# Performance work log

Hardware: AMD Instinct MI355X
Metric: run time of the kernel (lower is better)

## Reference

```python
import jax, jax.numpy as jnp
import numpy as np

N = 2_000_000   # num_nodes
C = 128         # in_channels
B = 256         # num graphs
K = 32          # max branches per graph (branch ids in [0, K))
NEG_SLOPE = 0.01  # torch leaky_relu default


def setup_inputs() -> dict:
    key = jax.random.key(0)
    k1, k2, k3, k4, k5, k6 = jax.random.split(key, 6)
    node_embed = jax.random.normal(k1, (N, C), dtype=jnp.float32)
    batch = jnp.sort(jax.random.randint(k2, (N,), 0, B, dtype=jnp.int64))
    branch = jax.random.randint(k3, (N,), 0, K, dtype=jnp.int64)
    s1 = 1.0 / np.sqrt(C)
    W1 = jax.random.uniform(k4, (C, C), jnp.float32, -s1, s1)
    b1 = jnp.zeros((C,), jnp.float32)
    W2 = jax.random.uniform(k5, (C, 1), jnp.float32, -s1, s1)
    b2 = jnp.zeros((1,), jnp.float32)
    return {"node_embed": node_embed, "batch": batch, "branch": branch,
            "W1": W1, "b1": b1, "W2": W2, "b2": b2}


def reference(node_embed, batch, branch, W1, b1, W2, b2):
    # Original code compacts branch ids via per-graph offsets (cumsum of max+1).
    # Equivalent static-shape formulation: global slot id = batch*K + branch,
    # and a per-graph mask keeping slots b <= max(branch in graph) — exactly the
    # branches 0..num_branch_per_graph-1 that repeat_interleave covers (including
    # empty branches below the max, whose pooled embed is 0 -> MLP(0)).
    gid = batch * K + branch                               # [N]
    branch_embed = jax.ops.segment_sum(node_embed, gid, num_segments=B * K)  # [B*K, C]
    h = branch_embed @ W1 + b1
    h = jnp.where(h >= 0, h, NEG_SLOPE * h)                # leaky_relu
    branch_value = h @ W2 + b2                             # [B*K, 1]
    max_b = jax.ops.segment_max(branch, batch, num_segments=B)  # [B]
    mask = (jnp.arange(K)[None, :] <= max_b[:, None]).astype(branch_value.dtype)  # [B, K]
    graph_value = jnp.sum(branch_value.reshape(B, K) * mask, axis=1, keepdims=True)  # [B, 1]
    return graph_value
```

## Files before the change

kernel.cpp:

```cpp
#include <hip/hip_runtime.h>

#define NCH 128
#define NGR 256
#define NBR 32
#define NEG_SLOPE 0.01f

typedef __attribute__((ext_vector_type(8))) short bf16x8;
typedef __attribute__((ext_vector_type(4))) float f32x4;

constexpr int TROWS = 128;

__device__ inline unsigned short f32_bf16(float x) {
    unsigned u = __float_as_uint(x);
    return (unsigned short)((u + 0x7FFFu + ((u >> 16) & 1u)) >> 16);
}
__device__ inline float bf16_f32(unsigned short h) {
    return __uint_as_float(((unsigned)h) << 16);
}

__global__ __launch_bounds__(1024) void scatter_mfma(
    const float* __restrict__ node_embed,
    const int*   __restrict__ batch,
    const int*   __restrict__ branch,
    float*       __restrict__ branch_embed,
    int*         __restrict__ max_b,
    int n_nodes)
{
    __shared__ float buf[2][TROWS][NCH] __attribute__((aligned(16)));
    __shared__ unsigned short sbr[2][TROWS] __attribute__((aligned(16)));
    __shared__ int seg_s[2];
    __shared__ int wm[2];

    const int t    = threadIdx.x;
    const int g    = blockIdx.x;
    const int wave = t >> 6;
    const int lane = t & 63;
    const int c    = wave >> 1;
    const int p    = wave & 1;

    if (t < 2) {
        const int target = g + t;
        int lo = 0, hi = n_nodes;
        while (lo < hi) { int mid = (lo + hi) >> 1; if (batch[mid] < target) lo = mid + 1; else hi = mid; }
        seg_s[t] = lo;
    }
    __syncthreads();
    const int s0 = seg_s[0], s1 = seg_s[1];
    const int nt = (s1 - s0 + TROWS - 1) / TROWS;

    auto stage_data = [&](int c0n, int nb) {
        #pragma unroll
        for (int u = 0; u < 4; ++u) {
            const int koff = (u * 16 + wave) * 1024;
            const size_t lanebyte = (size_t)koff + (size_t)lane * 16;
            const int rowg = c0n + (int)(lanebyte >> 9);
            const char* src = (const char*)node_embed + (((size_t)c0n << 9) + lanebyte);
            if (rowg >= s1)
                src = (const char*)node_embed + ((size_t)s0 << 9);
            __builtin_amdgcn_global_load_lds(
                (const __attribute__((address_space(1))) void*)src,
                (__attribute__((address_space(3))) void*)((char*)&buf[nb][0][0] + koff),
                16, 0, 0);
        }
    };

    f32x4 acc0 = {0.f, 0.f, 0.f, 0.f};
    f32x4 acc1 = {0.f, 0.f, 0.f, 0.f};
    int mymax = -1;

    if (nt > 0) {
        stage_data(s0, 0);
        if (t < TROWS) {
            const int i = s0 + t;
            unsigned short mm = 0xFFFFu;
            if (i < s1) { const int br = branch[i]; mymax = max(mymax, br); mm = (unsigned short)br; }
            sbr[0][t] = mm;
        }
        __syncthreads();
    }

    const int gq = lane >> 4;
    const int m  = lane & 15;

    for (int ti = 0; ti < nt; ++ti) {
        const int cb = ti & 1;
        const bool pre = (ti + 1 < nt);
        unsigned short nxt = 0xFFFFu;
        if (pre) {
            const int c0n = s0 + (ti + 1) * TROWS;
            stage_data(c0n, cb ^ 1);
            if (t < TROWS) {
                const int i = c0n + t;
                if (i < s1) { const int br = branch[i]; mymax = max(mymax, br); nxt = (unsigned short)br; }
            }
        }

        #pragma unroll
        for (int kk = 0; kk < 2; ++kk) {
            const int rb = (p + 2 * kk) * 32;
            const int4 idraw = *(const int4*)((const char*)&sbr[cb][0] + rb * 2 + gq * 16);
            unsigned idv[8];
            idv[0] = (unsigned)idraw.x & 0xFFFFu; idv[1] = (unsigned)idraw.x >> 16;
            idv[2] = (unsigned)idraw.y & 0xFFFFu; idv[3] = (unsigned)idraw.y >> 16;
            idv[4] = (unsigned)idraw.z & 0xFFFFu; idv[5] = (unsigned)idraw.z >> 16;
            idv[6] = (unsigned)idraw.w & 0xFFFFu; idv[7] = (unsigned)idraw.w >> 16;

            bf16x8 a0, a1, bhi, blo;
            #pragma unroll
            for (int j = 0; j < 8; ++j) {
                const float v = buf[cb][rb + gq * 8 + j][c * 16 + m];
                const unsigned short h = f32_bf16(v);
                const unsigned short l = f32_bf16(v - bf16_f32(h));
                bhi[j] = (short)h;
                blo[j] = (short)l;
                a0[j] = (idv[j] == (unsigned)m)        ? (short)0x3F80 : (short)0;
                a1[j] = (idv[j] == (unsigned)(m + 16)) ? (short)0x3F80 : (short)0;
            }
            acc0 = __builtin_amdgcn_mfma_f32_16x16x32_bf16(a0, bhi, acc0, 0, 0, 0);
            acc0 = __builtin_amdgcn_mfma_f32_16x16x32_bf16(a0, blo, acc0, 0, 0, 0);
            acc1 = __builtin_amdgcn_mfma_f32_16x16x32_bf16(a1, bhi, acc1, 0, 0, 0);
            acc1 = __builtin_amdgcn_mfma_f32_16x16x32_bf16(a1, blo, acc1, 0, 0, 0);
        }

        if (pre && t < TROWS) sbr[cb ^ 1][t] = nxt;
        __syncthreads();
    }

    __syncthreads();
    float* red = &buf[0][0][0];
    if (p == 1) {
        float* dst = red + ((size_t)c * 64 + lane) * 8;
        #pragma unroll
        for (int r = 0; r < 4; ++r) { dst[r] = acc0[r]; dst[4 + r] = acc1[r]; }
    }
    __syncthreads();
    if (p == 0) {
        const float* src = red + ((size_t)c * 64 + lane) * 8;
        #pragma unroll
        for (int r = 0; r < 4; ++r) { acc0[r] += src[r]; acc1[r] += src[4 + r]; }
        const int sr = gq * 4;
        float* be = branch_embed + (size_t)g * NBR * NCH + (size_t)c * 16 + m;
        #pragma unroll
        for (int r = 0; r < 4; ++r) {
            be[(sr + r) * NCH]      = acc0[r];
            be[(16 + sr + r) * NCH] = acc1[r];
        }
    }

    int v = mymax;
    #pragma unroll
    for (int off = 32; off > 0; off >>= 1) v = max(v, __shfl_down(v, off));
    if (wave < 2 && lane == 0) wm[wave] = v;
    __syncthreads();
    if (t == 0) max_b[g] = max(wm[0], wm[1]);
}

__global__ __launch_bounds__(256) void mlp_kernel(
    const float* __restrict__ branch_embed,
    const int*   __restrict__ max_b,
    const float* __restrict__ W1,
    const float* __restrict__ b1,
    const float* __restrict__ W2,
    const float* __restrict__ b2,
    float*       __restrict__ out)
{
    __shared__ float W1s[NCH * NCH];
    __shared__ float b1s[NCH], W2s[NCH];
    __shared__ float rows[2][NCH];
    __shared__ float red[2][NCH];
    __shared__ float sval[NBR];

    const int t = threadIdx.x;
    const int b = blockIdx.x;

    for (int i = t; i < NCH * NCH / 4; i += 256)
        ((float4*)W1s)[i] = ((const float4*)W1)[i];
    if (t < NCH) { b1s[t] = b1[t]; W2s[t] = W2[t]; }
    __syncthreads();

    const int half = t >> 7;
    const int j    = t & 127;

    for (int k0 = 0; k0 < NBR; k0 += 2) {
        const int slot = k0 + half;
        rows[half][j] = branch_embed[((size_t)b * NBR + slot) * NCH + j];
        __syncthreads();

        float h = b1s[j];
        #pragma unroll 8
        for (int i = 0; i < NCH; ++i)
            h += rows[half][i] * W1s[i * NCH + j];
        h = (h >= 0.0f) ? h : NEG_SLOPE * h;
        red[half][j] = h * W2s[j];
        __syncthreads();

        for (int off = 64; off > 0; off >>= 1) {
            if (j < off) red[half][j] += red[half][j + off];
            __syncthreads();
        }
        if (j == 0) sval[slot] = red[half][0];
        __syncthreads();
    }

    if (t < 64) {
        const int mb = max_b[b];
        float v = (t < NBR && t <= mb) ? (sval[t] + b2[0]) : 0.0f;
        #pragma unroll
        for (int off = 32; off > 0; off >>= 1) v += __shfl_down(v, off);
        if (t == 0) out[b] = v;
    }
}

extern "C" void kernel_launch(void* const* d_in, const int* in_sizes, int n_in,
                              void* d_out, int out_size, void* d_ws, size_t ws_size,
                              hipStream_t stream) {
    const float* node_embed = (const float*)d_in[0];
    const int*   batch      = (const int*)d_in[1];
    const int*   branch     = (const int*)d_in[2];
    const float* W1         = (const float*)d_in[3];
    const float* b1         = (const float*)d_in[4];
    const float* W2         = (const float*)d_in[5];
    const float* b2         = (const float*)d_in[6];
    float*       out        = (float*)d_out;

    const int n_nodes = in_sizes[0] / NCH;

    float* branch_embed = (float*)d_ws;
    int*   max_b = (int*)((char*)d_ws + (size_t)NGR * NBR * NCH * sizeof(float));

    scatter_mfma<<<NGR, 1024, 0, stream>>>(node_embed, batch, branch,
                                           branch_embed, max_b, n_nodes);
    mlp_kernel<<<NGR, 256, 0, stream>>>(branch_embed, max_b, W1, b1, W2, b2, out);
}
```

Before: 246.1 us.

## Deepen scatter pipeline to two tiles ahead with async branch-id loads

Restructures the scatter kernel's tile loop so two tiles are in flight. The branch ids are now also loaded straight into LDS with global_load_lds, and waits use explicit vmcnt counters and raw barriers instead of __syncthreads. The bf16 high part becomes a cheap truncation rather than round-to-nearest. Tail rows are masked in a templated compute path, and every wave folds the max branch into its own mymax. The aim is to hide global-load latency and cut per-tile register/ALU overhead. The cost is fragile hand-tuned waitcnt counts and some extra reduction work.

Result: faster. 235.9 us (-4.2%).

```diff
diff --git a/kernel.cpp b/kernel.cpp
--- a/kernel.cpp
+++ b/kernel.cpp
@@ -10,12 +10,49 @@
 
 constexpr int TROWS = 128;
 
-__device__ inline unsigned short f32_bf16(float x) {
+__device__ inline unsigned short rtne_bf16(float x) {
     unsigned u = __float_as_uint(x);
     return (unsigned short)((u + 0x7FFFu + ((u >> 16) & 1u)) >> 16);
 }
-__device__ inline float bf16_f32(unsigned short h) {
-    return __uint_as_float(((unsigned)h) << 16);
+
+template <bool TAIL>
+__device__ inline void compute_tile(
+    const float (*__restrict__ buf)[NCH], const int* __restrict__ sbr, int rem,
+    int p, int c, int gq, int m,
+    f32x4& acc0, f32x4& acc1, int& mymax)
+{
+    #pragma unroll
+    for (int kk = 0; kk < 2; ++kk) {
+        const int rb = (p + 2 * kk) * 32 + gq * 8;
+        int idv[8];
+        {
+            const int4 i0 = *(const int4*)&sbr[rb];
+            const int4 i1 = *(const int4*)&sbr[rb + 4];
+            idv[0] = i0.x; idv[1] = i0.y; idv[2] = i0.z; idv[3] = i0.w;
+            idv[4] = i1.x; idv[5] = i1.y; idv[6] = i1.z; idv[7] = i1.w;
+        }
+        bf16x8 a0, a1, bhi, blo;
+        #pragma unroll
+        for (int j = 0; j < 8; ++j) {
+            const float v = buf[rb + j][c * 16 + m];
+            const unsigned u = __float_as_uint(v);
+            const unsigned short h = (unsigned short)(u >> 16);
+            const float hf = __uint_as_float(u & 0xFFFF0000u);
+            const unsigned short l = rtne_bf16(v - hf);
+            bhi[j] = (short)h;
+            blo[j] = (short)l;
+            bool val = true;
+            if (TAIL) val = (rb + j) < rem;
+            a0[j] = (val && idv[j] == m)      ? (short)0x3F80 : (short)0;
+            a1[j] = (val && idv[j] == m + 16) ? (short)0x3F80 : (short)0;
+            if (TAIL) { if (val) mymax = max(mymax, idv[j]); }
+            else      mymax = max(mymax, idv[j]);
+        }
+        acc0 = __builtin_amdgcn_mfma_f32_16x16x32_bf16(a0, bhi, acc0, 0, 0, 0);
+        acc0 = __builtin_amdgcn_mfma_f32_16x16x32_bf16(a0, blo, acc0, 0, 0, 0);
+        acc1 = __builtin_amdgcn_mfma_f32_16x16x32_bf16(a1, bhi, acc1, 0, 0, 0);
+        acc1 = __builtin_amdgcn_mfma_f32_16x16x32_bf16(a1, blo, acc1, 0, 0, 0);
+    }
 }
 
 __global__ __launch_bounds__(1024) void scatter_mfma(
@@ -27,9 +64,9 @@
     int n_nodes)
 {
     __shared__ float buf[2][TROWS][NCH] __attribute__((aligned(16)));
-    __shared__ unsigned short sbr[2][TROWS] __attribute__((aligned(16)));
-    __shared__ int seg_s[2];
-    __shared__ int wm[2];
+    __shared__ int   sbr_i[2][TROWS]    __attribute__((aligned(16)));
+    __shared__ int   seg_s[2];
+    __shared__ int   wm[16];
 
     const int t    = threadIdx.x;
     const int g    = blockIdx.x;
@@ -37,6 +74,8 @@
     const int lane = t & 63;
     const int c    = wave >> 1;
     const int p    = wave & 1;
+    const int gq   = lane >> 4;
+    const int m    = lane & 15;
 
     if (t < 2) {
         const int target = g + t;
@@ -48,7 +87,9 @@
     const int s0 = seg_s[0], s1 = seg_s[1];
     const int nt = (s1 - s0 + TROWS - 1) / TROWS;
 
-    auto stage_data = [&](int c0n, int nb) {
+    auto stage = [&](int ti2) {
+        const int c0n = s0 + ti2 * TROWS;
+        const int nb  = ti2 & 1;
         #pragma unroll
         for (int u = 0; u < 4; ++u) {
             const int koff = (u * 16 + wave) * 1024;
@@ -62,6 +103,16 @@
                 (__attribute__((address_space(3))) void*)((char*)&buf[nb][0][0] + koff),
                 16, 0, 0);
         }
+        if (wave == 0) {
+            const int i0 = min(c0n + lane,      n_nodes - 1);
+            const int i1 = min(c0n + 64 + lane, n_nodes - 1);
+            __builtin_amdgcn_global_load_lds(
+                (const __attribute__((address_space(1))) void*)(branch + i0),
+                (__attribute__((address_space(3))) void*)((char*)&sbr_i[nb][0]), 4, 0, 0);
+            __builtin_amdgcn_global_load_lds(
+                (const __attribute__((address_space(1))) void*)(branch + i1),
+                (__attribute__((address_space(3))) void*)((char*)&sbr_i[nb][0] + 256), 4, 0, 0);
+        }
     };
 
     f32x4 acc0 = {0.f, 0.f, 0.f, 0.f};
@@ -69,61 +120,42 @@
     int mymax = -1;
 
     if (nt > 0) {
-        stage_data(s0, 0);
-        if (t < TROWS) {
-            const int i = s0 + t;
-            unsigned short mm = 0xFFFFu;
-            if (i < s1) { const int br = branch[i]; mymax = max(mymax, br); mm = (unsigned short)br; }
-            sbr[0][t] = mm;
-        }
-        __syncthreads();
-    }
-
-    const int gq = lane >> 4;
-    const int m  = lane & 15;
-
-    for (int ti = 0; ti < nt; ++ti) {
-        const int cb = ti & 1;
-        const bool pre = (ti + 1 < nt);
-        unsigned short nxt = 0xFFFFu;
-        if (pre) {
-            const int c0n = s0 + (ti + 1) * TROWS;
-            stage_data(c0n, cb ^ 1);
-            if (t < TROWS) {
-                const int i = c0n + t;
-                if (i < s1) { const int br = branch[i]; mymax = max(mymax, br); nxt = (unsigned short)br; }
+        stage(0);
+        if (nt > 1) stage(1);
+        if (nt > 1) {
+            if (wave == 0) asm volatile("s_waitcnt vmcnt(6)" ::: "memory");
+            else           asm volatile("s_waitcnt vmcnt(4)" ::: "memory");
+        } else {
+            asm volatile("s_waitcnt vmcnt(0)" ::: "memory");
+        }
+        __builtin_amdgcn_s_barrier();
+        __builtin_amdgcn_sched_barrier(0);
+
+        for (int ti = 0; ti < nt; ++ti) {
+            const int cb = ti & 1;
+            if (ti == nt - 1)
+                compute_tile<true >(buf[cb], sbr_i[cb], s1 - (s0 + ti * TROWS),
+                                    p, c, gq, m, acc0, acc1, mymax);
+            else
+                compute_tile<false>(buf[cb], sbr_i[cb], 0,
+                                    p, c, gq, m, acc0, acc1, mymax);
+
+            __builtin_amdgcn_s_barrier();
+            __builtin_amdgcn_sched_barrier(0);
+
+            const bool more = (ti + 2 < nt);
+            if (more) stage(ti + 2);
+            if (ti + 1 < nt) {
+                if (more) {
+                    if (wave == 0) asm volatile("s_waitcnt vmcnt(6)" ::: "memory");
+                    else           asm volatile("s_waitcnt vmcnt(4)" ::: "memory");
+                } else {
+                    asm volatile("s_waitcnt vmcnt(0)" ::: "memory");
+                }
+                __builtin_amdgcn_s_barrier();
+                __builtin_amdgcn_sched_barrier(0);
             }
         }
-
-        #pragma unroll
-        for (int kk = 0; kk < 2; ++kk) {
-            const int rb = (p + 2 * kk) * 32;
-            const int4 idraw = *(const int4*)((const char*)&sbr[cb][0] + rb * 2 + gq * 16);
-            unsigned idv[8];
-            idv[0] = (unsigned)idraw.x & 0xFFFFu; idv[1] = (unsigned)idraw.x >> 16;
-            idv[2] = (unsigned)idraw.y & 0xFFFFu; idv[3] = (unsigned)idraw.y >> 16;
-            idv[4] = (unsigned)idraw.z & 0xFFFFu; idv[5] = (unsigned)idraw.z >> 16;
-            idv[6] = (unsigned)idraw.w & 0xFFFFu; idv[7] = (unsigned)idraw.w >> 16;
-
-            bf16x8 a0, a1, bhi, blo;
-            #pragma unroll
-            for (int j = 0; j < 8; ++j) {
-                const float v = buf[cb][rb + gq * 8 + j][c * 16 + m];
-                const unsigned short h = f32_bf16(v);
-                const unsigned short l = f32_bf16(v - bf16_f32(h));
-                bhi[j] = (short)h;
-                blo[j] = (short)l;
-                a0[j] = (idv[j] == (unsigned)m)        ? (short)0x3F80 : (short)0;
-                a1[j] = (idv[j] == (unsigned)(m + 16)) ? (short)0x3F80 : (short)0;
-            }
-            acc0 = __builtin_amdgcn_mfma_f32_16x16x32_bf16(a0, bhi, acc0, 0, 0, 0);
-            acc0 = __builtin_amdgcn_mfma_f32_16x16x32_bf16(a0, blo, acc0, 0, 0, 0);
-            acc1 = __builtin_amdgcn_mfma_f32_16x16x32_bf16(a1, bhi, acc1, 0, 0, 0);
-            acc1 = __builtin_amdgcn_mfma_f32_16x16x32_bf16(a1, blo, acc1, 0, 0, 0);
-        }
-
-        if (pre && t < TROWS) sbr[cb ^ 1][t] = nxt;
-        __syncthreads();
     }
 
     __syncthreads();
@@ -150,9 +182,14 @@
     int v = mymax;
     #pragma unroll
     for (int off = 32; off > 0; off >>= 1) v = max(v, __shfl_down(v, off));
-    if (wave < 2 && lane == 0) wm[wave] = v;
-    __syncthreads();
-    if (t == 0) max_b[g] = max(wm[0], wm[1]);
+    if (lane == 0) wm[wave] = v;
+    __syncthreads();
+    if (t == 0) {
+        int mb = wm[0];
+        #pragma unroll
+        for (int i = 1; i < 16; ++i) mb = max(mb, wm[i]);
+        max_b[g] = mb;
+    }
 }
 
 __global__ __launch_bounds__(256) void mlp_kernel(
```
